# Performance work log

Measured on AMD Instinct MI355X. Metric: run time of the kernel, lower is better.

Reference implementation:

```python
import jax, jax.numpy as jnp
import numpy as np

H = 16
D_MODEL = 1024
D_K = D_MODEL // H


def setup_inputs() -> dict:
    key = jax.random.key(0)
    ks = jax.random.split(key, 10)
    B, S = 2, 2048
    q = jax.random.normal(ks[0], (B, S, D_MODEL), dtype=jnp.float32)
    k = jax.random.normal(ks[1], (B, S, D_MODEL), dtype=jnp.float32)
    v = jax.random.normal(ks[2], (B, S, D_MODEL), dtype=jnp.float32)
    mask = jax.random.randint(ks[3], (B, 1, S), 0, 2, dtype=jnp.int32)
    s = 1.0 / np.sqrt(D_MODEL)
    w_q = jax.random.normal(ks[4], (D_MODEL, D_MODEL), dtype=jnp.float32) * s
    b_q = jnp.zeros((D_MODEL,), dtype=jnp.float32)
    w_v = jax.random.normal(ks[5], (D_MODEL, D_MODEL), dtype=jnp.float32) * s
    b_v = jnp.zeros((D_MODEL,), dtype=jnp.float32)
    w_o = jax.random.normal(ks[6], (D_MODEL, D_MODEL), dtype=jnp.float32) * s
    b_o = jnp.zeros((D_MODEL,), dtype=jnp.float32)
    return {"q": q, "k": k, "v": v, "mask": mask,
            "w_q": w_q, "b_q": b_q, "w_v": w_v, "b_v": b_v,
            "w_o": w_o, "b_o": b_o}


def _split_heads(x, B):
    # [B, S, D] -> [B, H, S, d_k]
    return x.reshape(B, -1, H, D_K).transpose(0, 2, 1, 3)


def reference(q, k, v, mask, w_q, b_q, w_v, b_v, w_o, b_o):
    B = q.shape[0]
    # NOTE: source uses w_q for BOTH q and k (w_k is dead code) — reproduced faithfully.
    qh = _split_heads(q @ w_q.T + b_q, B)
    kh = _split_heads(k @ w_q.T + b_q, B)
    vh = _split_heads(v @ w_v.T + b_v, B)
    scores = jnp.einsum('bhqd,bhkd->bhqk', qh, kh) * (1.0 / np.sqrt(D_K))
    # mask [B,1,S] -> unsqueeze(1) -> [B,1,1,S], broadcast over heads and query dim
    m = mask[:, None, :, :]
    scores = jnp.where(m == 0, -jnp.inf, scores)
    attn = jax.nn.softmax(scores, axis=-1)  # dropout is identity (eval / p=0)
    out = jnp.einsum('bhqk,bhkd->bhqd', attn, vh)
    out = out.transpose(0, 2, 1, 3).reshape(B, -1, D_MODEL)
    out = out @ w_o.T + b_o
    return out, attn
```

## Files before the change

kernel.cpp:

```cpp
#include <hip/hip_runtime.h>

#define S_LEN 2048
#define DMODEL 1024
#define NH 16
#define DK 64
#define BATCH 2
#define BS (BATCH * S_LEN)
#define KHALF 1024

typedef _Float16 f16;
typedef _Float16 f16x8 __attribute__((ext_vector_type(8)));
typedef _Float16 f16x4 __attribute__((ext_vector_type(4)));
typedef float f32x4 __attribute__((ext_vector_type(4)));

__device__ __forceinline__ f32x4 mfma16(f16x8 a, f16x8 b, f32x4 c) {
  return __builtin_amdgcn_mfma_f32_16x16x32_f16(a, b, c, 0, 0, 0);
}

__global__ __launch_bounds__(256) void cvt6(
    const float* __restrict__ a0, const float* __restrict__ a1,
    const float* __restrict__ a2, const float* __restrict__ a3,
    const float* __restrict__ a4, const float* __restrict__ a5,
    f16* __restrict__ d0, f16* __restrict__ d1, f16* __restrict__ d2,
    f16* __restrict__ d3, f16* __restrict__ d4, f16* __restrict__ d5) {
  const int y = blockIdx.y;
  const float* s;
  f16* d;
  switch (y) {
    case 0: s = a0; d = d0; break;
    case 1: s = a1; d = d1; break;
    case 2: s = a2; d = d2; break;
    case 3: s = a3; d = d3; break;
    case 4: s = a4; d = d4; break;
    default: s = a5; d = d5; break;
  }
  const int n = (y < 3) ? BS * DMODEL : DMODEL * DMODEL;
  const int idx = (blockIdx.x * 256 + threadIdx.x) * 4;
  if (idx >= n) return;
  const float4 v = *reinterpret_cast<const float4*>(&s[idx]);
  f16x4 h = {(f16)v.x, (f16)v.y, (f16)v.z, (f16)v.w};
  *reinterpret_cast<f16x4*>(&d[idx]) = h;
}

template <int MODE>
__device__ __forceinline__ void gemm_body16(const f16* __restrict__ A,
                                            const f16* __restrict__ W,
                                            const float* __restrict__ bias,
                                            void* __restrict__ outp, float scale,
                                            f16 (*As)[72], f16 (*Ws)[72]) {
  const int t = threadIdx.x;
  const int m0 = blockIdx.y * 128;
  const int n0 = blockIdx.x * 128;
  const int wave = t >> 6, lane = t & 63;
  const int wr = wave >> 1, wc = wave & 1;
  const int lcol = lane & 15, kq = lane >> 4;

  f32x4 acc[4][4];
  const f32x4 zero = {0.f, 0.f, 0.f, 0.f};
#pragma unroll
  for (int i = 0; i < 4; ++i)
#pragma unroll
    for (int j = 0; j < 4; ++j) acc[i][j] = zero;

  for (int k0 = 0; k0 < DMODEL; k0 += 64) {
#pragma unroll
    for (int i = 0; i < 4; ++i) {
      const int f = t + i * 256;
      const int r = f >> 3, c = (f & 7) << 3;
      *reinterpret_cast<f16x8*>(&As[r][c]) =
          *reinterpret_cast<const f16x8*>(&A[(size_t)(m0 + r) * DMODEL + k0 + c]);
      *reinterpret_cast<f16x8*>(&Ws[r][c]) =
          *reinterpret_cast<const f16x8*>(&W[(size_t)(n0 + r) * DMODEL + k0 + c]);
    }
    __syncthreads();
#pragma unroll
    for (int ks = 0; ks < 2; ++ks) {
      f16x8 af[4], bf[4];
#pragma unroll
      for (int fr = 0; fr < 4; ++fr)
        af[fr] = *reinterpret_cast<const f16x8*>(
            &As[wr * 64 + fr * 16 + lcol][ks * 32 + kq * 8]);
#pragma unroll
      for (int fc = 0; fc < 4; ++fc)
        bf[fc] = *reinterpret_cast<const f16x8*>(
            &Ws[wc * 64 + fc * 16 + lcol][ks * 32 + kq * 8]);
#pragma unroll
      for (int fr = 0; fr < 4; ++fr)
#pragma unroll
        for (int fc = 0; fc < 4; ++fc)
          acc[fr][fc] = mfma16(af[fr], bf[fc], acc[fr][fc]);
    }
    __syncthreads();
  }

#pragma unroll
  for (int fc = 0; fc < 4; ++fc) {
    const int gj = n0 + wc * 64 + fc * 16 + lcol;
    const float bv = bias[gj];
#pragma unroll
    for (int fr = 0; fr < 4; ++fr) {
#pragma unroll
      for (int r = 0; r < 4; ++r) {
        const int gi = m0 + wr * 64 + fr * 16 + kq * 4 + r;
        const float val = (acc[fr][fc][r] + bv) * scale;
        if constexpr (MODE == 0) {
          const int b = gi >> 11, s = gi & 2047, h = gj >> 6, dk = gj & 63;
          ((f16*)outp)[(((size_t)(b * NH + h) * S_LEN) + s) * DK + dk] = (f16)val;
        } else if constexpr (MODE == 1) {
          const int b = gi >> 11, s = gi & 2047, h = gj >> 6, dk = gj & 63;
          ((f16*)outp)[(((size_t)(b * NH + h) * DK) + dk) * S_LEN + s] = (f16)val;
        } else {
          ((float*)outp)[(size_t)gi * DMODEL + gj] = val;
        }
      }
    }
  }
}

__global__ __launch_bounds__(256, 3) void qkv_gemm(
    const f16* __restrict__ qf, const f16* __restrict__ kf,
    const f16* __restrict__ vf, const f16* __restrict__ wq,
    const float* __restrict__ b_q, const f16* __restrict__ wv,
    const float* __restrict__ b_v, f16* __restrict__ qh, f16* __restrict__ kh,
    f16* __restrict__ vhT) {
  __shared__ f16 As[128][72];
  __shared__ f16 Ws[128][72];
  if (blockIdx.z == 0)
    gemm_body16<0>(qf, wq, b_q, qh, 0.125f, As, Ws);
  else if (blockIdx.z == 1)
    gemm_body16<0>(kf, wq, b_q, kh, 1.0f, As, Ws);
  else
    gemm_body16<1>(vf, wv, b_v, vhT, 1.0f, As, Ws);
}

__global__ __launch_bounds__(256, 2) void gemm_out(const f16* __restrict__ A,
                                                   const f16* __restrict__ W,
                                                   const float* __restrict__ bias,
                                                   float* __restrict__ outp) {
  __shared__ f16 As[128][72];
  __shared__ f16 Ws[128][72];
  gemm_body16<2>(A, W, bias, outp, 1.0f, As, Ws);
}

__global__ __launch_bounds__(256, 4) void attn_fused(
    const f16* __restrict__ qh, const f16* __restrict__ kh,
    const f16* __restrict__ vhT, const int* __restrict__ mask,
    float* __restrict__ attn, f16* __restrict__ ctx) {
  __shared__ __align__(16) unsigned char smem[18432];
  const int t = threadIdx.x;
  const int bh = blockIdx.y, b = bh >> 4, h = bh & 15;
  const int i0 = blockIdx.x * 64;
  const int wave = t >> 6, lane = t & 63;
  const int rh = wave & 1, khf = wave >> 1;
  const int lcol = lane & 15, kq = lane >> 4;
  const int rbase = i0 + rh * 32;
  const int jbase = khf * KHALF;
  f16 (*Ps)[72] = reinterpret_cast<f16(*)[72]>(smem + wave * 4608);
  float (*Ost)[68] = reinterpret_cast<float(*)[68]>(smem);
  float* lred = reinterpret_cast<float*>(smem + 17408);

  const f16* Q = qh + (size_t)bh * S_LEN * DK;
  const f16* K = kh + (size_t)bh * S_LEN * DK;
  const f16* V = vhT + (size_t)bh * DK * S_LEN;
  const int* msk = mask + b * S_LEN;
  float* Sc = attn + (size_t)bh * S_LEN * S_LEN;

  f16x8 aq[2][2];
#pragma unroll
  for (int rt = 0; rt < 2; ++rt)
#pragma unroll
    for (int ks = 0; ks < 2; ++ks)
      aq[rt][ks] = *reinterpret_cast<const f16x8*>(
          &Q[(size_t)(rbase + rt * 16 + lcol) * DK + ks * 32 + kq * 8]);

  float l_acc[2][4];
  f32x4 o[2][4];
  const f32x4 zero = {0.f, 0.f, 0.f, 0.f};
#pragma unroll
  for (int rt = 0; rt < 2; ++rt) {
#pragma unroll
    for (int r = 0; r < 4; ++r) l_acc[rt][r] = 0.f;
#pragma unroll
    for (int d = 0; d < 4; ++d) o[rt][d] = zero;
  }

  for (int j0 = jbase; j0 < jbase + KHALF; j0 += 64) {
#pragma unroll
    for (int jt = 0; jt < 4; ++jt) {
      const f16* Krow = &K[(size_t)(j0 + jt * 16 + lcol) * DK + kq * 8];
      const f16x8 bk0 = *reinterpret_cast<const f16x8*>(Krow);
      const f16x8 bk1 = *reinterpret_cast<const f16x8*>(Krow + 32);
      const int mv = msk[j0 + jt * 16 + lcol];
#pragma unroll
      for (int rt = 0; rt < 2; ++rt) {
        f32x4 c = zero;
        c = mfma16(aq[rt][0], bk0, c);
        c = mfma16(aq[rt][1], bk1, c);
#pragma unroll
        for (int r = 0; r < 4; ++r) {
          const float pun = mv ? __expf(c[r]) : 0.f;
          l_acc[rt][r] += pun;
          Ps[rt * 16 + kq * 4 + r][jt * 16 + lcol] = (f16)pun;
        }
      }
    }
#pragma unroll
    for (int ks = 0; ks < 2; ++ks) {
      f16x8 ap[2], bv[4];
#pragma unroll
      for (int rt = 0; rt < 2; ++rt)
        ap[rt] = *reinterpret_cast<const f16x8*>(
            &Ps[rt * 16 + lcol][ks * 32 + kq * 8]);
#pragma unroll
      for (int d = 0; d < 4; ++d)
        bv[d] = *reinterpret_cast<const f16x8*>(
            &V[(size_t)(d * 16 + lcol) * S_LEN + j0 + ks * 32 + kq * 8]);
#pragma unroll
      for (int rt = 0; rt < 2; ++rt)
#pragma unroll
        for (int d = 0; d < 4; ++d) o[rt][d] = mfma16(ap[rt], bv[d], o[rt][d]);
    }
  }

#pragma unroll
  for (int rt = 0; rt < 2; ++rt)
#pragma unroll
    for (int r = 0; r < 4; ++r) {
      float es = l_acc[rt][r];
#pragma unroll
      for (int off = 1; off < 16; off <<= 1) es += __shfl_xor(es, off);
      l_acc[rt][r] = es;
    }

  __syncthreads();

  if (lcol == 0) {
#pragma unroll
    for (int rt = 0; rt < 2; ++rt)
#pragma unroll
      for (int r = 0; r < 4; ++r)
        lred[khf * 64 + rh * 32 + rt * 16 + kq * 4 + r] = l_acc[rt][r];
  }
  if (khf == 1) {
#pragma unroll
    for (int rt = 0; rt < 2; ++rt)
#pragma unroll
      for (int d = 0; d < 4; ++d)
#pragma unroll
        for (int r = 0; r < 4; ++r)
          Ost[rh * 32 + rt * 16 + kq * 4 + r][d * 16 + lcol] = o[rt][d][r];
  }
  __syncthreads();

  float il[2][4];
#pragma unroll
  for (int rt = 0; rt < 2; ++rt)
#pragma unroll
    for (int r = 0; r < 4; ++r) {
      const int rl = rh * 32 + rt * 16 + kq * 4 + r;
      il[rt][r] = 1.0f / (lred[rl] + lred[64 + rl]);
    }

  for (int j0 = jbase; j0 < jbase + KHALF; j0 += 64) {
#pragma unroll
    for (int jt = 0; jt < 4; ++jt) {
      const f16* Krow = &K[(size_t)(j0 + jt * 16 + lcol) * DK + kq * 8];
      const f16x8 bk0 = *reinterpret_cast<const f16x8*>(Krow);
      const f16x8 bk1 = *reinterpret_cast<const f16x8*>(Krow + 32);
      const int mv = msk[j0 + jt * 16 + lcol];
#pragma unroll
      for (int rt = 0; rt < 2; ++rt) {
        f32x4 c = zero;
        c = mfma16(aq[rt][0], bk0, c);
        c = mfma16(aq[rt][1], bk1, c);
#pragma unroll
        for (int r = 0; r < 4; ++r) {
          const float p = mv ? __expf(c[r]) * il[rt][r] : 0.f;
          Sc[((size_t)(rbase + rt * 16 + kq * 4 + r) << 11) + j0 + jt * 16 +
             lcol] = p;
        }
      }
    }
  }

  if (khf == 0) {
#pragma unroll
    for (int rt = 0; rt < 2; ++rt)
#pragma unroll
      for (int d = 0; d < 4; ++d) {
        const int dk = d * 16 + lcol;
#pragma unroll
        for (int r = 0; r < 4; ++r) {
          const int rl = rh * 32 + rt * 16 + kq * 4 + r;
          const float ov = o[rt][d][r] + Ost[rl][dk];
          const int s = rbase + rt * 16 + kq * 4 + r;
          ctx[(size_t)(b * S_LEN + s) * DMODEL + h * DK + dk] =
              (f16)(ov * il[rt][r]);
        }
      }
  }
}

extern "C" void kernel_launch(void* const* d_in, const int* in_sizes, int n_in,
                              void* d_out, int out_size, void* d_ws, size_t ws_size,
                              hipStream_t stream) {
  const float* q = (const float*)d_in[0];
  const float* k = (const float*)d_in[1];
  const float* v = (const float*)d_in[2];
  const int* mask = (const int*)d_in[3];
  const float* w_q = (const float*)d_in[4];
  const float* b_q = (const float*)d_in[5];
  const float* w_v = (const float*)d_in[6];
  const float* b_v = (const float*)d_in[7];
  const float* w_o = (const float*)d_in[8];
  const float* b_o = (const float*)d_in[9];

  float* out = (float*)d_out;
  float* attn = out + (size_t)BS * DMODEL;

  f16* qf = (f16*)d_ws;
  f16* kf = qf + (size_t)BS * DMODEL;
  f16* vf = kf + (size_t)BS * DMODEL;
  f16* wqf = vf + (size_t)BS * DMODEL;
  f16* wvf = wqf + (size_t)DMODEL * DMODEL;
  f16* wof = wvf + (size_t)DMODEL * DMODEL;
  f16* qh = wof + (size_t)DMODEL * DMODEL;
  f16* kh = qh + (size_t)BS * DMODEL;
  f16* vhT = kh + (size_t)BS * DMODEL;
  f16* ctx = vhT + (size_t)BS * DMODEL;

  cvt6<<<dim3(4096, 6), 256, 0, stream>>>(q, k, v, w_q, w_v, w_o, qf, kf, vf,
                                          wqf, wvf, wof);
  qkv_gemm<<<dim3(8, 32, 3), 256, 0, stream>>>(qf, kf, vf, wqf, b_q, wvf, b_v,
                                               qh, kh, vhT);
  attn_fused<<<dim3(32, 32), 256, 0, stream>>>(qh, kh, vhT, mask, attn, ctx);
  gemm_out<<<dim3(8, 32), 256, 0, stream>>>(ctx, wof, b_o, out);
}
```

Baseline: 932.3 us.

## Transpose QK MFMA operands to keep P in registers and vectorize attn stores

Swaps the A/B operands of the QK^T MFMA so each lane holds four consecutive key columns of one query row. The P tile can then be packed straight into the PV MFMA A operand in registers, with no LDS staging through Ps. The mask is now loaded as int4 and the attention-probability writes become float4 stores along rows, replacing scalar strided stores. The V loads become two f16x4 loads with a reordered k index. Row-sum reduction shrinks to two shuffles, and one barrier is removed.

```diff
diff --git a/kernel.cpp b/kernel.cpp
--- a/kernel.cpp
+++ b/kernel.cpp
@@ -146,7 +146,7 @@
     const f16* __restrict__ qh, const f16* __restrict__ kh,
     const f16* __restrict__ vhT, const int* __restrict__ mask,
     float* __restrict__ attn, f16* __restrict__ ctx) {
-  __shared__ __align__(16) unsigned char smem[18432];
+  __shared__ __align__(16) unsigned char smem[17920];
   const int t = threadIdx.x;
   const int bh = blockIdx.y, b = bh >> 4, h = bh & 15;
   const int i0 = blockIdx.x * 64;
@@ -155,7 +155,6 @@
   const int lcol = lane & 15, kq = lane >> 4;
   const int rbase = i0 + rh * 32;
   const int jbase = khf * KHALF;
-  f16 (*Ps)[72] = reinterpret_cast<f16(*)[72]>(smem + wave * 4608);
   float (*Ost)[68] = reinterpret_cast<float(*)[68]>(smem);
   float* lred = reinterpret_cast<float*>(smem + 17408);
 
@@ -173,15 +172,92 @@
       aq[rt][ks] = *reinterpret_cast<const f16x8*>(
           &Q[(size_t)(rbase + rt * 16 + lcol) * DK + ks * 32 + kq * 8]);
 
-  float l_acc[2][4];
+  float l_acc[2] = {0.f, 0.f};
   f32x4 o[2][4];
   const f32x4 zero = {0.f, 0.f, 0.f, 0.f};
 #pragma unroll
+  for (int rt = 0; rt < 2; ++rt)
+#pragma unroll
+    for (int d = 0; d < 4; ++d) o[rt][d] = zero;
+
+  for (int j0 = jbase; j0 < jbase + KHALF; j0 += 64) {
+#pragma unroll
+    for (int jh = 0; jh < 2; ++jh) {
+      f16x8 ap[2];
+#pragma unroll
+      for (int jl = 0; jl < 2; ++jl) {
+        const int jt = jh * 2 + jl;
+        const f16* Krow = &K[(size_t)(j0 + jt * 16 + lcol) * DK + kq * 8];
+        const f16x8 bk0 = *reinterpret_cast<const f16x8*>(Krow);
+        const f16x8 bk1 = *reinterpret_cast<const f16x8*>(Krow + 32);
+        const int4 m4 =
+            *reinterpret_cast<const int4*>(&msk[j0 + jt * 16 + kq * 4]);
+#pragma unroll
+        for (int rt = 0; rt < 2; ++rt) {
+          f32x4 c = zero;
+          c = mfma16(bk0, aq[rt][0], c);
+          c = mfma16(bk1, aq[rt][1], c);
+          const float p0 = m4.x ? __expf(c[0]) : 0.f;
+          const float p1 = m4.y ? __expf(c[1]) : 0.f;
+          const float p2 = m4.z ? __expf(c[2]) : 0.f;
+          const float p3 = m4.w ? __expf(c[3]) : 0.f;
+          l_acc[rt] += (p0 + p1) + (p2 + p3);
+          ap[rt][jl * 4 + 0] = (f16)p0;
+          ap[rt][jl * 4 + 1] = (f16)p1;
+          ap[rt][jl * 4 + 2] = (f16)p2;
+          ap[rt][jl * 4 + 3] = (f16)p3;
+        }
+      }
+#pragma unroll
+      for (int d = 0; d < 4; ++d) {
+        const f16* Vr =
+            &V[(size_t)(d * 16 + lcol) * S_LEN + j0 + jh * 32 + kq * 4];
+        const f16x4 v0 = *reinterpret_cast<const f16x4*>(Vr);
+        const f16x4 v1 = *reinterpret_cast<const f16x4*>(Vr + 16);
+        f16x8 bv;
+        bv[0] = v0[0]; bv[1] = v0[1]; bv[2] = v0[2]; bv[3] = v0[3];
+        bv[4] = v1[0]; bv[5] = v1[1]; bv[6] = v1[2]; bv[7] = v1[3];
+#pragma unroll
+        for (int rt = 0; rt < 2; ++rt) o[rt][d] = mfma16(ap[rt], bv, o[rt][d]);
+      }
+    }
+  }
+
+#pragma unroll
   for (int rt = 0; rt < 2; ++rt) {
-#pragma unroll
-    for (int r = 0; r < 4; ++r) l_acc[rt][r] = 0.f;
-#pragma unroll
-    for (int d = 0; d < 4; ++d) o[rt][d] = zero;
+    float es = l_acc[rt];
+    es += __shfl_xor(es, 16);
+    es += __shfl_xor(es, 32);
+    l_acc[rt] = es;
+  }
+
+  if (kq == 0) {
+#pragma unroll
+    for (int rt = 0; rt < 2; ++rt)
+      lred[khf * 64 + rh * 32 + rt * 16 + lcol] = l_acc[rt];
+  }
+  if (khf == 1) {
+#pragma unroll
+    for (int rt = 0; rt < 2; ++rt)
+#pragma unroll
+      for (int d = 0; d < 4; ++d)
+#pragma unroll
+        for (int r = 0; r < 4; ++r)
+          Ost[rh * 32 + rt * 16 + kq * 4 + r][d * 16 + lcol] = o[rt][d][r];
+  }
+  __syncthreads();
+
+  float ile[2][4];
+  float il2[2];
+#pragma unroll
+  for (int rt = 0; rt < 2; ++rt) {
+#pragma unroll
+    for (int r = 0; r < 4; ++r) {
+      const int rl = rh * 32 + rt * 16 + kq * 4 + r;
+      ile[rt][r] = 1.0f / (lred[rl] + lred[64 + rl]);
+    }
+    const int rl2 = rh * 32 + rt * 16 + lcol;
+    il2[rt] = 1.0f / (lred[rl2] + lred[64 + rl2]);
   }
 
   for (int j0 = jbase; j0 < jbase + KHALF; j0 += 64) {
@@ -190,95 +266,21 @@
       const f16* Krow = &K[(size_t)(j0 + jt * 16 + lcol) * DK + kq * 8];
       const f16x8 bk0 = *reinterpret_cast<const f16x8*>(Krow);
       const f16x8 bk1 = *reinterpret_cast<const f16x8*>(Krow + 32);
-      const int mv = msk[j0 + jt * 16 + lcol];
+      const int4 m4 =
+          *reinterpret_cast<const int4*>(&msk[j0 + jt * 16 + kq * 4]);
 #pragma unroll
       for (int rt = 0; rt < 2; ++rt) {
         f32x4 c = zero;
-        c = mfma16(aq[rt][0], bk0, c);
-        c = mfma16(aq[rt][1], bk1, c);
-#pragma unroll
-        for (int r = 0; r < 4; ++r) {
-          const float pun = mv ? __expf(c[r]) : 0.f;
-          l_acc[rt][r] += pun;
-          Ps[rt * 16 + kq * 4 + r][jt * 16 + lcol] = (f16)pun;
-        }
-      }
-    }
-#pragma unroll
-    for (int ks = 0; ks < 2; ++ks) {
-      f16x8 ap[2], bv[4];
-#pragma unroll
-      for (int rt = 0; rt < 2; ++rt)
-        ap[rt] = *reinterpret_cast<const f16x8*>(
-            &Ps[rt * 16 + lcol][ks * 32 + kq * 8]);
-#pragma unroll
-      for (int d = 0; d < 4; ++d)
-        bv[d] = *reinterpret_cast<const f16x8*>(
-            &V[(size_t)(d * 16 + lcol) * S_LEN + j0 + ks * 32 + kq * 8]);
-#pragma unroll
-      for (int rt = 0; rt < 2; ++rt)
-#pragma unroll
-        for (int d = 0; d < 4; ++d) o[rt][d] = mfma16(ap[rt], bv[d], o[rt][d]);
-    }
-  }
-
-#pragma unroll
-  for (int rt = 0; rt < 2; ++rt)
-#pragma unroll
-    for (int r = 0; r < 4; ++r) {
-      float es = l_acc[rt][r];
-#pragma unroll
-      for (int off = 1; off < 16; off <<= 1) es += __shfl_xor(es, off);
-      l_acc[rt][r] = es;
-    }
-
-  __syncthreads();
-
-  if (lcol == 0) {
-#pragma unroll
-    for (int rt = 0; rt < 2; ++rt)
-#pragma unroll
-      for (int r = 0; r < 4; ++r)
-        lred[khf * 64 + rh * 32 + rt * 16 + kq * 4 + r] = l_acc[rt][r];
-  }
-  if (khf == 1) {
-#pragma unroll
-    for (int rt = 0; rt < 2; ++rt)
-#pragma unroll
-      for (int d = 0; d < 4; ++d)
-#pragma unroll
-        for (int r = 0; r < 4; ++r)
-          Ost[rh * 32 + rt * 16 + kq * 4 + r][d * 16 + lcol] = o[rt][d][r];
-  }
-  __syncthreads();
-
-  float il[2][4];
-#pragma unroll
-  for (int rt = 0; rt < 2; ++rt)
-#pragma unroll
-    for (int r = 0; r < 4; ++r) {
-      const int rl = rh * 32 + rt * 16 + kq * 4 + r;
-      il[rt][r] = 1.0f / (lred[rl] + lred[64 + rl]);
-    }
-
-  for (int j0 = jbase; j0 < jbase + KHALF; j0 += 64) {
-#pragma unroll
-    for (int jt = 0; jt < 4; ++jt) {
-      const f16* Krow = &K[(size_t)(j0 + jt * 16 + lcol) * DK + kq * 8];
-      const f16x8 bk0 = *reinterpret_cast<const f16x8*>(Krow);
-      const f16x8 bk1 = *reinterpret_cast<const f16x8*>(Krow + 32);
-      const int mv = msk[j0 + jt * 16 + lcol];
-#pragma unroll
-      for (int rt = 0; rt < 2; ++rt) {
-        f32x4 c = zero;
-        c = mfma16(aq[rt][0], bk0, c);
-        c = mfma16(aq[rt][1], bk1, c);
-#pragma unroll
-        for (int r = 0; r < 4; ++r) {
-          const float p = mv ? __expf(c[r]) * il[rt][r] : 0.f;
-          Sc[((size_t)(rbase + rt * 16 + kq * 4 + r) << 11) + j0 + jt * 16 +
-             lcol] = p;
-        }
+        c = mfma16(bk0, aq[rt][0], c);
+        c = mfma16(bk1, aq[rt][1], c);
+        float4 st;
+        st.x = m4.x ? __expf(c[0]) * il2[rt] : 0.f;
+        st.y = m4.y ? __expf(c[1]) * il2[rt] : 0.f;
+        st.z = m4.z ? __expf(c[2]) * il2[rt] : 0.f;
+        st.w = m4.w ? __expf(c[3]) * il2[rt] : 0.f;
+        *reinterpret_cast<float4*>(
+            &Sc[((size_t)(rbase + rt * 16 + lcol) << 11) + j0 + jt * 16 +
+                kq * 4]) = st;
       }
     }
   }
@@ -295,7 +297,7 @@
           const float ov = o[rt][d][r] + Ost[rl][dk];
           const int s = rbase + rt * 16 + kq * 4 + r;
           ctx[(size_t)(b * S_LEN + s) * DMODEL + h * DK + dk] =
-              (f16)(ov * il[rt][r]);
+              (f16)(ov * ile[rt][r]);
         }
       }
   }
```

New measurement: 1.035 ms. 11.0% more time.
